# Kernel tuning notes

Measured on AMD Instinct MI355X. Metric: run time of the kernel, lower is better.

Reference implementation:

```python
import jax, jax.numpy as jnp
import numpy as np

DIM = 1024
NUM_HEADS = 16
HEAD_DIM = DIM // NUM_HEADS


def setup_inputs() -> dict:
    key = jax.random.key(0)
    k1, k2, k3, k4, k5 = jax.random.split(key, 5)
    B, N = 4, 2048
    x = jax.random.normal(k1, (B, N, DIM), dtype=jnp.float32)
    s_in = 1.0 / np.sqrt(DIM)
    W_qkv = jax.random.normal(k2, (DIM, 3 * DIM), dtype=jnp.float32) * s_in
    b_qkv = jax.random.normal(k3, (3 * DIM,), dtype=jnp.float32) * 0.02
    W_proj = jax.random.normal(k4, (DIM, DIM), dtype=jnp.float32) * s_in
    b_proj = jax.random.normal(k5, (DIM,), dtype=jnp.float32) * 0.02
    return {"x": x, "W_qkv": W_qkv, "b_qkv": b_qkv, "W_proj": W_proj, "b_proj": b_proj}


def reference(x, W_qkv, b_qkv, W_proj, b_proj):
    B, N, C = x.shape
    H, D = NUM_HEADS, HEAD_DIM
    scale = D ** -0.5
    qkv = x @ W_qkv + b_qkv                      # [B, N, 3C]
    qkv = qkv.reshape(B, N, 3, H, D)
    q = jnp.transpose(qkv[:, :, 0], (0, 2, 1, 3))  # [B, H, N, D]
    k = jnp.transpose(qkv[:, :, 1], (0, 2, 1, 3))
    v = jnp.transpose(qkv[:, :, 2], (0, 2, 1, 3))
    # scaled dot-product attention (dropout_p=0 in eval)
    attn = jnp.einsum("bhqd,bhkd->bhqk", q, k) * scale
    attn = jax.nn.softmax(attn, axis=-1)
    o = jnp.einsum("bhqk,bhkd->bhqd", attn, v)   # [B, H, N, D]
    o = jnp.transpose(o, (0, 2, 1, 3)).reshape(B, N, C)
    return o @ W_proj + b_proj
```

## Files before the change

### kernel.cpp

```cpp
#include <hip/hip_runtime.h>
#include <hip/hip_bf16.h>
#include <cstdint>

#define DIMC 1024
#define NHEAD 16
#define HD 64
#define SEQ 2048
#define NTOK 8192

typedef __attribute__((ext_vector_type(8))) short bfrag;
typedef __attribute__((ext_vector_type(4))) short spack4;
typedef __attribute__((ext_vector_type(4))) float fv4;
typedef __attribute__((ext_vector_type(16))) float f32x16;
typedef __attribute__((ext_vector_type(4))) int iv4;

static __device__ __forceinline__ unsigned short f2bf(float f) {
  union { float f; unsigned int u; } v; v.f = f;
  return (unsigned short)((v.u + 0x7fffu + ((v.u >> 16) & 1u)) >> 16);
}
static __device__ __forceinline__ unsigned int pack2c(float a, float b) {
  __hip_bfloat16 ha(a), hb(b);
  unsigned short ua, ub;
  __builtin_memcpy(&ua, &ha, 2);
  __builtin_memcpy(&ub, &hb, 2);
  return (unsigned int)ua | ((unsigned int)ub << 16);
}

#define MFMA(a, b, c) __builtin_amdgcn_mfma_f32_16x16x32_bf16((a), (b), (c), 0, 0, 0)
#define MFMA32(a, b, c) __builtin_amdgcn_mfma_f32_32x32x16_bf16((a), (b), (c), 0, 0, 0)

#define GLOAD_LDS(gp, lp)                                                  \
  __builtin_amdgcn_global_load_lds(                                        \
      (const __attribute__((address_space(1))) void*)(gp),                 \
      (__attribute__((address_space(3))) void*)(lp), 16, 0, 0)

__global__ void prep(const float* __restrict__ x, short* __restrict__ xb,
                     const float* __restrict__ Wqkv, short* __restrict__ WqT,
                     const float* __restrict__ Wproj, short* __restrict__ WpT) {
  __shared__ float tile[32][33];
  const int bid = blockIdx.x;
  const int t = threadIdx.x;
  if (bid < 8192) {
    int i = (bid * 256 + t) * 4;
    fv4 v = *(const fv4*)&x[i];
    spack4 o;
#pragma unroll
    for (int j = 0; j < 4; ++j) o[j] = (short)f2bf(v[j]);
    *(spack4*)&xb[i] = o;
    return;
  }
  const float* W; short* WT; int R, C, bx, by;
  if (bid < 11264) { W = Wqkv; WT = WqT; R = 1024; C = 3072;
                     bx = (bid - 8192) % 96; by = (bid - 8192) / 96; }
  else             { W = Wproj; WT = WpT; R = 1024; C = 1024;
                     bx = (bid - 11264) % 32; by = (bid - 11264) / 32; }
  const int r = t >> 3, c4 = t & 7;
  const int r0 = by * 32, c0 = bx * 32;
  fv4 v = *(const fv4*)&W[(size_t)(r0 + r) * C + c0 + c4 * 4];
#pragma unroll
  for (int j = 0; j < 4; ++j) tile[r][c4 * 4 + j] = v[j];
  __syncthreads();
  spack4 o;
#pragma unroll
  for (int j = 0; j < 4; ++j) o[j] = (short)f2bf(tile[c4 * 4 + j][r]);
  *(spack4*)&WT[(size_t)(c0 + r) * R + r0 + c4 * 4] = o;
}

template <int MODE>
__launch_bounds__(256)
__global__ void gemm_bt(const short* __restrict__ A, const short* __restrict__ BT,
                        const float* __restrict__ bias, int M, int N, int K,
                        short* __restrict__ out0, short* __restrict__ out1,
                        short* __restrict__ out2, float* __restrict__ outf) {
  __shared__ alignas(16) char As[128 * 128];
  __shared__ alignas(16) char Bs[128 * 128];
  const int t = threadIdx.x;
  const int lane = t & 63;
  const int wid = t >> 6;
  const int wm = wid >> 1, wn = wid & 1;
  const int g = lane >> 4, l15 = lane & 15;
  const int row0 = blockIdx.y * 128;
  const int col0 = blockIdx.x * 128;

  fv4 acc[4][4] = {};

  const int srow = t >> 3;
  const int sk = (((t & 7) ^ (srow & 7)) * 8);

  for (int k0 = 0; k0 < K; k0 += 64) {
#pragma unroll
    for (int i = 0; i < 4; ++i) {
      const int row = i * 32 + srow;
      GLOAD_LDS(&A[(size_t)(row0 + row) * K + k0 + sk], &As[i * 4096 + t * 16]);
      GLOAD_LDS(&BT[(size_t)(col0 + row) * K + k0 + sk], &Bs[i * 4096 + t * 16]);
    }
    __syncthreads();
#pragma unroll
    for (int kk = 0; kk < 2; ++kk) {
      bfrag af[4], bf[4];
#pragma unroll
      for (int mm = 0; mm < 4; ++mm) {
        int row = wm * 64 + mm * 16 + l15;
        af[mm] = *(const bfrag*)&As[row * 128 + ((kk * 64 + g * 16) ^ ((row & 7) << 4))];
      }
#pragma unroll
      for (int nn = 0; nn < 4; ++nn) {
        int row = wn * 64 + nn * 16 + l15;
        bf[nn] = *(const bfrag*)&Bs[row * 128 + ((kk * 64 + g * 16) ^ ((row & 7) << 4))];
      }
#pragma unroll
      for (int mm = 0; mm < 4; ++mm)
#pragma unroll
        for (int nn = 0; nn < 4; ++nn)
          acc[mm][nn] = MFMA(af[mm], bf[nn], acc[mm][nn]);
    }
    __syncthreads();
  }

  if (MODE == 0) {
    const float qs = 0.125f * 1.4426950408889634f;
#pragma unroll
    for (int nn = 0; nn < 4; ++nn) {
      int col = col0 + wn * 64 + nn * 16 + l15;
      int which = col >> 10;
      int rem = col & 1023;
      int h = rem >> 6, d = rem & 63;
      float bval = bias[col];
#pragma unroll
      for (int mm = 0; mm < 4; ++mm) {
        int tok = row0 + wm * 64 + mm * 16 + g * 4;
        int b = tok >> 11, n = tok & 2047;
        int bh = b * NHEAD + h;
        if (which == 0) {
#pragma unroll
          for (int r = 0; r < 4; ++r)
            out0[((size_t)bh * SEQ + n + r) * HD + d] =
                (short)f2bf((acc[mm][nn][r] + bval) * qs);
        } else if (which == 1) {
#pragma unroll
          for (int r = 0; r < 4; ++r)
            out1[((size_t)bh * SEQ + n + r) * HD + d] =
                (short)f2bf(acc[mm][nn][r] + bval);
        } else {
          int n2 = (n & ~15) | ((n & 4) << 1) | ((n & 8) >> 1);
          spack4 p;
#pragma unroll
          for (int r = 0; r < 4; ++r) p[r] = (short)f2bf(acc[mm][nn][r] + bval);
          *(spack4*)&out2[((size_t)bh * HD + d) * SEQ + n2] = p;
        }
      }
    }
  } else {
#pragma unroll
    for (int nn = 0; nn < 4; ++nn) {
      int col = col0 + wn * 64 + nn * 16 + l15;
      float bval = bias[col];
#pragma unroll
      for (int mm = 0; mm < 4; ++mm) {
        int tok = row0 + wm * 64 + mm * 16 + g * 4;
#pragma unroll
        for (int r = 0; r < 4; ++r)
          outf[(size_t)(tok + r) * N + col] = acc[mm][nn][r] + bval;
      }
    }
  }
}

__launch_bounds__(256, 2)
__global__ void attn_fwd(const short* __restrict__ Q, const short* __restrict__ Kb,
                         const short* __restrict__ VT, short* __restrict__ O) {
  __shared__ alignas(16) char Ks[2][8192];
  __shared__ alignas(16) char Vs[2][8192];

  const int t = threadIdx.x, lane = t & 63, wid = t >> 6;
  const int l31 = lane & 31, hi = lane >> 5;
  const int rsw = (l31 & 7) << 4;

  const int bid = blockIdx.x;
  const int xcd = bid & 7, mm_ = bid >> 3;
  const int bh = xcd + 8 * (mm_ >> 3);
  const int qt = mm_ & 7;

  const size_t base = (size_t)bh * SEQ * HD;
  const short* Qp = Q + base;
  const short* Kp = Kb + base;
  const short* Vp = VT + base;
  const int q0 = qt * 256 + wid * 32;
  const int q1 = q0 + 128;

  bfrag qfA[4], qfB[4];
#pragma unroll
  for (int dblk = 0; dblk < 4; ++dblk) {
    qfA[dblk] = *(const bfrag*)&Qp[(size_t)(q0 + l31) * HD + dblk * 16 + hi * 8];
    qfB[dblk] = *(const bfrag*)&Qp[(size_t)(q1 + l31) * HD + dblk * 16 + hi * 8];
  }

  bfrag ones;
#pragma unroll
  for (int j = 0; j < 8; ++j) ones[j] = (short)0x3F80;

  f32x16 oaccA[2] = {}, oaccB[2] = {};
  f32x16 laccA = {}, laccB = {};

  const int sr = t >> 3, ss = t & 7;
  const int swz0 = (ss * 16) ^ ((sr & 7) << 4);

  {
    bfrag k0 = *(const bfrag*)&Kp[(size_t)sr * HD + ss * 8];
    bfrag k1 = *(const bfrag*)&Kp[(size_t)(32 + sr) * HD + ss * 8];
    bfrag v0 = *(const bfrag*)&Vp[(size_t)sr * SEQ + ss * 8];
    bfrag v1 = *(const bfrag*)&Vp[(size_t)(sr + 32) * SEQ + ss * 8];
    *(bfrag*)&Ks[0][sr * 128 + swz0] = k0;
    *(bfrag*)&Ks[0][(sr + 32) * 128 + swz0] = k1;
    *(bfrag*)&Vs[0][sr * 128 + swz0] = v0;
    *(bfrag*)&Vs[0][(sr + 32) * 128 + swz0] = v1;
  }
  __syncthreads();

  int cur = 0;
  for (int kt = 0; kt < SEQ / 64; ++kt) {
    bfrag nk0, nk1, nv0, nv1;
    const bool pre = (kt + 1) < (SEQ / 64);
    if (pre) {
      const int kb2 = (kt + 1) * 64;
      nk0 = *(const bfrag*)&Kp[(size_t)(kb2 + sr) * HD + ss * 8];
      nk1 = *(const bfrag*)&Kp[(size_t)(kb2 + 32 + sr) * HD + ss * 8];
      nv0 = *(const bfrag*)&Vp[(size_t)sr * SEQ + kb2 + ss * 8];
      nv1 = *(const bfrag*)&Vp[(size_t)(sr + 32) * SEQ + kb2 + ss * 8];
    }

    const char* Kc = Ks[cur];
    const char* Vc = Vs[cur];

    f32x16 sA0 = {}, sA1 = {}, sB0 = {}, sB1 = {};
    __builtin_amdgcn_s_setprio(1);
#pragma unroll
    for (int dblk = 0; dblk < 4; ++dblk) {
      const int c = (dblk * 32 + hi * 16) ^ rsw;
      bfrag kf0 = *(const bfrag*)&Kc[l31 * 128 + c];
      bfrag kf1 = *(const bfrag*)&Kc[(32 + l31) * 128 + c];
      sA0 = MFMA32(kf0, qfA[dblk], sA0);
      sB0 = MFMA32(kf0, qfB[dblk], sB0);
      sA1 = MFMA32(kf1, qfA[dblk], sA1);
      sB1 = MFMA32(kf1, qfB[dblk], sB1);
    }

#pragma unroll
    for (int hb = 0; hb < 4; ++hb) {
      const int ob = (hb & 1) * 8;
      const f32x16 vA = (hb >> 1) ? sA1 : sA0;
      const f32x16 vB = (hb >> 1) ? sB1 : sB0;
      float eA[8], eB[8];
#pragma unroll
      for (int i = 0; i < 8; ++i) {
        eA[i] = __builtin_amdgcn_exp2f(vA[ob + i]);
        eB[i] = __builtin_amdgcn_exp2f(vB[ob + i]);
      }
      iv4 ia, ib;
#pragma unroll
      for (int w = 0; w < 4; ++w) {
        ia[w] = (int)pack2c(eA[2 * w], eA[2 * w + 1]);
        ib[w] = (int)pack2c(eB[2 * w], eB[2 * w + 1]);
      }
      const bfrag pbA = __builtin_bit_cast(bfrag, ia);
      const bfrag pbB = __builtin_bit_cast(bfrag, ib);
      laccA = MFMA32(ones, pbA, laccA);
      laccB = MFMA32(ones, pbB, laccB);
#pragma unroll
      for (int dh = 0; dh < 2; ++dh) {
        const int row = dh * 32 + l31;
        bfrag vf = *(const bfrag*)&Vc[row * 128 + ((hb * 32 + hi * 16) ^ rsw)];
        oaccA[dh] = MFMA32(vf, pbA, oaccA[dh]);
        oaccB[dh] = MFMA32(vf, pbB, oaccB[dh]);
      }
    }
    __builtin_amdgcn_s_setprio(0);

    if (pre) {
      const int nb = cur ^ 1;
      *(bfrag*)&Ks[nb][sr * 128 + swz0] = nk0;
      *(bfrag*)&Ks[nb][(sr + 32) * 128 + swz0] = nk1;
      *(bfrag*)&Vs[nb][sr * 128 + swz0] = nv0;
      *(bfrag*)&Vs[nb][(sr + 32) * 128 + swz0] = nv1;
      __syncthreads();
    }
    cur ^= 1;
  }

  const float invA = 1.0f / laccA[0];
  const float invB = 1.0f / laccB[0];
  const int b = bh >> 4, h = bh & 15;
#pragma unroll
  for (int dh = 0; dh < 2; ++dh)
#pragma unroll
    for (int gp = 0; gp < 4; ++gp) {
      const int d0 = dh * 32 + gp * 8 + hi * 4;
      spack4 pkA, pkB;
#pragma unroll
      for (int j = 0; j < 4; ++j) {
        pkA[j] = (short)f2bf(oaccA[dh][gp * 4 + j] * invA);
        pkB[j] = (short)f2bf(oaccB[dh][gp * 4 + j] * invB);
      }
      *(spack4*)&O[((size_t)b * SEQ + (q0 + l31)) * DIMC + h * HD + d0] = pkA;
      *(spack4*)&O[((size_t)b * SEQ + (q1 + l31)) * DIMC + h * HD + d0] = pkB;
    }
}

extern "C" void kernel_launch(void* const* d_in, const int* in_sizes, int n_in,
                              void* d_out, int out_size, void* d_ws, size_t ws_size,
                              hipStream_t stream) {
  const float* x     = (const float*)d_in[0];
  const float* Wqkv  = (const float*)d_in[1];
  const float* bqkv  = (const float*)d_in[2];
  const float* Wproj = (const float*)d_in[3];
  const float* bproj = (const float*)d_in[4];
  float* out = (float*)d_out;
  char* ws = (char*)d_ws;

  short* xb  = (short*)(ws);
  short* WqT = (short*)(ws + 16777216);
  short* WpT = (short*)(ws + 23068672);
  short* Qb  = (short*)(ws + 25165824);
  short* Kb  = (short*)(ws + 41943040);
  short* VTb = (short*)(ws + 58720256);
  short* Ob  = (short*)(ws + 75497472);

  prep<<<12288, 256, 0, stream>>>(x, xb, Wqkv, WqT, Wproj, WpT);
  gemm_bt<0><<<dim3(24, 64), 256, 0, stream>>>(xb, WqT, bqkv, NTOK, 3072, 1024,
                                               Qb, Kb, VTb, nullptr);
  attn_fwd<<<512, 256, 0, stream>>>(Qb, Kb, VTb, Ob);
  gemm_bt<1><<<dim3(8, 64), 256, 0, stream>>>(Ob, WpT, bproj, NTOK, 1024, 1024,
                                              nullptr, nullptr, nullptr, out);
}
```

Before: 186.6 us.

## Stage attention K/V tiles via direct global-to-LDS loads with smaller blocks

Replaces the register-staged K/V prefetch in the attention kernel with direct global-to-LDS loads (GLOAD_LDS), using a pre-swizzled source address so the LDS layout stays conflict-free. The block shrinks to 128 threads covering 128 queries, and the grid doubles to 1024 blocks. This removes the register round trip and the explicit LDS stores, freeing VGPRs and raising block count for occupancy. The trade-off is more total K/V traffic per head, since each tile is now shared by fewer queries. There is also reliance on a GLOAD_LDS macro defined elsewhere, with the sync placed just before the buffer swap.

```diff
diff --git a/kernel.cpp b/kernel.cpp
--- a/kernel.cpp
+++ b/kernel.cpp
@@ -166,7 +166,7 @@
   }
 }
 
-__launch_bounds__(256, 2)
+__launch_bounds__(128, 2)
 __global__ void attn_fwd(const short* __restrict__ Q, const short* __restrict__ Kb,
                          const short* __restrict__ VT, short* __restrict__ O) {
   __shared__ alignas(16) char Ks[2][8192];
@@ -178,15 +178,15 @@
 
   const int bid = blockIdx.x;
   const int xcd = bid & 7, mm_ = bid >> 3;
-  const int bh = xcd + 8 * (mm_ >> 3);
-  const int qt = mm_ & 7;
+  const int bh = xcd + 8 * (mm_ >> 4);
+  const int qt = mm_ & 15;
 
   const size_t base = (size_t)bh * SEQ * HD;
   const short* Qp = Q + base;
   const short* Kp = Kb + base;
   const short* Vp = VT + base;
-  const int q0 = qt * 256 + wid * 32;
-  const int q1 = q0 + 128;
+  const int q0 = qt * 128 + wid * 32;
+  const int q1 = q0 + 64;
 
   bfrag qfA[4], qfB[4];
 #pragma unroll
@@ -202,32 +202,26 @@
   f32x16 oaccA[2] = {}, oaccB[2] = {};
   f32x16 laccA = {}, laccB = {};
 
-  const int sr = t >> 3, ss = t & 7;
-  const int swz0 = (ss * 16) ^ ((sr & 7) << 4);
-
-  {
-    bfrag k0 = *(const bfrag*)&Kp[(size_t)sr * HD + ss * 8];
-    bfrag k1 = *(const bfrag*)&Kp[(size_t)(32 + sr) * HD + ss * 8];
-    bfrag v0 = *(const bfrag*)&Vp[(size_t)sr * SEQ + ss * 8];
-    bfrag v1 = *(const bfrag*)&Vp[(size_t)(sr + 32) * SEQ + ss * 8];
-    *(bfrag*)&Ks[0][sr * 128 + swz0] = k0;
-    *(bfrag*)&Ks[0][(sr + 32) * 128 + swz0] = k1;
-    *(bfrag*)&Vs[0][sr * 128 + swz0] = v0;
-    *(bfrag*)&Vs[0][(sr + 32) * 128 + swz0] = v1;
-  }
+  const int srow = t >> 3;
+  const int scx = ((t & 7) ^ (srow & 7)) * 8;
+
+#define STAGE_TILE(buf, kb)                                                \
+  _Pragma("unroll")                                                        \
+  for (int i = 0; i < 4; ++i) {                                            \
+    const int row_ = i * 16 + srow;                                        \
+    GLOAD_LDS(&Kp[(size_t)((kb) + row_) * HD + scx],                       \
+              &Ks[buf][i * 2048 + t * 16]);                                \
+    GLOAD_LDS(&Vp[(size_t)row_ * SEQ + (kb) + scx],                        \
+              &Vs[buf][i * 2048 + t * 16]);                                \
+  }
+
+  STAGE_TILE(0, 0)
   __syncthreads();
 
   int cur = 0;
   for (int kt = 0; kt < SEQ / 64; ++kt) {
-    bfrag nk0, nk1, nv0, nv1;
     const bool pre = (kt + 1) < (SEQ / 64);
-    if (pre) {
-      const int kb2 = (kt + 1) * 64;
-      nk0 = *(const bfrag*)&Kp[(size_t)(kb2 + sr) * HD + ss * 8];
-      nk1 = *(const bfrag*)&Kp[(size_t)(kb2 + 32 + sr) * HD + ss * 8];
-      nv0 = *(const bfrag*)&Vp[(size_t)sr * SEQ + kb2 + ss * 8];
-      nv1 = *(const bfrag*)&Vp[(size_t)(sr + 32) * SEQ + kb2 + ss * 8];
-    }
+    if (pre) STAGE_TILE(cur ^ 1, (kt + 1) * 64)
 
     const char* Kc = Ks[cur];
     const char* Vc = Vs[cur];
@@ -276,16 +270,10 @@
     }
     __builtin_amdgcn_s_setprio(0);
 
-    if (pre) {
-      const int nb = cur ^ 1;
-      *(bfrag*)&Ks[nb][sr * 128 + swz0] = nk0;
-      *(bfrag*)&Ks[nb][(sr + 32) * 128 + swz0] = nk1;
-      *(bfrag*)&Vs[nb][sr * 128 + swz0] = nv0;
-      *(bfrag*)&Vs[nb][(sr + 32) * 128 + swz0] = nv1;
-      __syncthreads();
-    }
+    if (pre) __syncthreads();
     cur ^= 1;
   }
+#undef STAGE_TILE
 
   const float invA = 1.0f / laccA[0];
   const float invB = 1.0f / laccB[0];
@@ -328,7 +316,7 @@
   prep<<<12288, 256, 0, stream>>>(x, xb, Wqkv, WqT, Wproj, WpT);
   gemm_bt<0><<<dim3(24, 64), 256, 0, stream>>>(xb, WqT, bqkv, NTOK, 3072, 1024,
                                                Qb, Kb, VTb, nullptr);
-  attn_fwd<<<512, 256, 0, stream>>>(Qb, Kb, VTb, Ob);
+  attn_fwd<<<1024, 128, 0, stream>>>(Qb, Kb, VTb, Ob);
   gemm_bt<1><<<dim3(8, 64), 256, 0, stream>>>(Ob, WpT, bproj, NTOK, 1024, 1024,
                                               nullptr, nullptr, nullptr, out);
 }
```

Measured after the change: 192.3 us. +3.0%, slower.
